# Kernel optimization log

Measured on AMD Instinct MI355X. Metric: run time of the kernel, lower is better.

The kernel has to match this reference:

```python
import jax, jax.numpy as jnp
import numpy as np


def setup_inputs() -> dict:
    key = jax.random.key(0)
    kx, kw = jax.random.split(key)
    x = jax.random.normal(kx, (32, 4096, 1024), dtype=jnp.float32)
    # torch init is rand*0.01 (all-positive, degenerate for sign); use randn*0.01
    # to emulate a trained BNN weight with mixed signs.
    weight = jax.random.normal(kw, (1024, 1024), dtype=jnp.float32) * 0.01
    return {"x": x, "weight": weight}


def reference(x, weight):
    # SignFunction forward: binarize weight to {-1, 0(+at exact 0), +1};
    # torch.sign semantics -> jnp.sign. F.linear(x, W) = x @ W.T
    b_weight = jnp.sign(weight)  # [out, in]
    return jnp.einsum('bsi,oi->bso', x, b_weight)
```

## Files before the change

### kernel.cpp

```cpp
#include <hip/hip_runtime.h>
#include <hip/hip_bf16.h>


typedef __attribute__((ext_vector_type(8))) short bf16x8;
typedef __attribute__((ext_vector_type(4))) float f32x4;

#define BM 128
#define BN 256
#define BK 32
#define KDIM 1024
#define NDIM 1024
#define NKSTEP (KDIM / BK)
#define PADA 40

__device__ __forceinline__ unsigned cvt2(float a, float b) {
  unsigned r;
  asm("v_cvt_pk_bf16_f32 %0, %1, %2" : "=v"(r) : "v"(a), "v"(b));
  return r;
}

__global__ void sign_kernel(const float4* __restrict__ W, ushort4* __restrict__ Bs, int n4) {
  int i = blockIdx.x * blockDim.x + threadIdx.x;
  if (i >= n4) return;
  float4 v = W[i];
  const float* pv = (const float*)&v;
  ushort4 r;
  unsigned short* pr = (unsigned short*)&r;
#pragma unroll
  for (int j = 0; j < 4; ++j) {
    union { float f; unsigned int u; } c; c.f = pv[j];
    pr[j] = ((c.u & 0x7fffffffu) == 0u)
                ? (unsigned short)0
                : (unsigned short)(0x3f80u | ((c.u >> 16) & 0x8000u));
  }
  Bs[i] = r;
}

__global__ __launch_bounds__(256) void bgemm_kernel(
    const float* __restrict__ X,
    const unsigned short* __restrict__ Bs,
    float* __restrict__ O) {
  __shared__ unsigned short sA[2][BM * PADA];
  __shared__ unsigned short sB[2][BN * BK];

  const int t = threadIdx.x;
  const int l = t & 63;
  const int w = t >> 6;
  const int wr = w >> 1;
  const int wc = w & 1;

  const unsigned nwg = gridDim.x;
  unsigned swz = blockIdx.x;
  if ((nwg & 7u) == 0u) swz = (blockIdx.x & 7u) * (nwg >> 3) + (blockIdx.x >> 3);
  const int bm = (int)(swz >> 2);
  const int bn = (int)(swz & 3u);
  const size_t m0 = (size_t)bm * BM;
  const int N0 = bn * BN;

  const int ar = t >> 1;
  const int ah = (t & 1) * 16;
  const float* ag = X + (m0 + (size_t)ar) * KDIM + ah;
  const int aw = ar * PADA + ah;

  const unsigned short* bg[4];
  int bw[4];
#pragma unroll
  for (int i = 0; i < 4; ++i) {
    int c = i * 256 + t;
    int n = c >> 2;
    int q = c & 3;
    int kb2 = q ^ ((n >> 1) & 3);
    bg[i] = Bs + (size_t)(N0 + n) * KDIM + kb2 * 8;
    bw[i] = c * 8;
  }

  const int ll = l & 15;
  const int kb = l >> 4;
  int offA[4], offB[8];
#pragma unroll
  for (int i = 0; i < 4; ++i)
    offA[i] = (wr * 64 + i * 16 + ll) * PADA + kb * 8;
#pragma unroll
  for (int j = 0; j < 8; ++j) {
    int n = wc * 128 + j * 16 + ll;
    int q = kb ^ ((n >> 1) & 3);
    offB[j] = n * BK + q * 8;
  }

  f32x4 acc[4][8];
#pragma unroll
  for (int i = 0; i < 4; ++i)
#pragma unroll
    for (int j = 0; j < 8; ++j) acc[i][j] = (f32x4)0.0f;

#define STAGE(buf, k0)                                                         \
  do {                                                                         \
    _Pragma("unroll") for (int i = 0; i < 4; ++i)                              \
        __builtin_amdgcn_global_load_lds(                                      \
            (const __attribute__((address_space(1))) void*)(bg[i] + (k0)),     \
            (__attribute__((address_space(3))) void*)(&sB[buf][bw[i]]),        \
            16, 0, 0);                                                         \
    const float4* ap = reinterpret_cast<const float4*>(ag + (k0));             \
    float4 v0 = ap[0], v1 = ap[1], v2 = ap[2], v3 = ap[3];                     \
    uint4 lo, hi;                                                              \
    lo.x = cvt2(v0.x, v0.y); lo.y = cvt2(v0.z, v0.w);                          \
    lo.z = cvt2(v1.x, v1.y); lo.w = cvt2(v1.z, v1.w);                          \
    hi.x = cvt2(v2.x, v2.y); hi.y = cvt2(v2.z, v2.w);                          \
    hi.z = cvt2(v3.x, v3.y); hi.w = cvt2(v3.z, v3.w);                          \
    *reinterpret_cast<uint4*>(&sA[buf][aw]) = lo;                              \
    *reinterpret_cast<uint4*>(&sA[buf][aw + 8]) = hi;                          \
  } while (0)

  STAGE(0, 0);
  __syncthreads();

  for (int kk = 0; kk < NKSTEP; ++kk) {
    const int cur = kk & 1;
    if (kk + 1 < NKSTEP) {
      STAGE(cur ^ 1, (kk + 1) * BK);
    }
    const unsigned short* sa = sA[cur];
    const unsigned short* sb = sB[cur];
    bf16x8 av[4];
    bf16x8 bv[8];
#pragma unroll
    for (int i = 0; i < 4; ++i)
      av[i] = *reinterpret_cast<const bf16x8*>(sa + offA[i]);
#pragma unroll
    for (int j = 0; j < 8; ++j)
      bv[j] = *reinterpret_cast<const bf16x8*>(sb + offB[j]);
#pragma unroll
    for (int i = 0; i < 4; ++i)
#pragma unroll
      for (int j = 0; j < 8; ++j)
        acc[i][j] = __builtin_amdgcn_mfma_f32_16x16x32_bf16(av[i], bv[j], acc[i][j], 0, 0, 0);
    __syncthreads();
  }

  const int crow = (l >> 4) * 4;
#pragma unroll
  for (int i = 0; i < 4; ++i) {
    const size_t r0 = m0 + wr * 64 + i * 16 + crow;
#pragma unroll
    for (int j = 0; j < 8; ++j) {
      const int col = N0 + wc * 128 + j * 16 + ll;
      float* op = O + r0 * NDIM + col;
#pragma unroll
      for (int e = 0; e < 4; ++e) op[(size_t)e * NDIM] = acc[i][j][e];
    }
  }
#undef STAGE
}

__global__ void naive_kernel(const float* __restrict__ X, const float* __restrict__ W,
                             float* __restrict__ O, long long total) {
  long long idx = (long long)blockIdx.x * blockDim.x + threadIdx.x;
  if (idx >= total) return;
  int n = (int)(idx & (NDIM - 1));
  long long m = idx >> 10;
  const float* xr = X + m * KDIM;
  const float* wr = W + (long long)n * KDIM;
  float s = 0.f;
  for (int k = 0; k < KDIM; ++k) {
    float wv = wr[k];
    float sg = (wv > 0.f) ? 1.f : ((wv < 0.f) ? -1.f : 0.f);
    s += xr[k] * sg;
  }
  O[idx] = s;
}

extern "C" void kernel_launch(void* const* d_in, const int* in_sizes, int n_in,
                              void* d_out, int out_size, void* d_ws, size_t ws_size,
                              hipStream_t stream) {
  const float* X = (const float*)d_in[0];
  const float* W = (const float*)d_in[1];
  float* O = (float*)d_out;
  const long long M = (long long)in_sizes[0] / KDIM;

  const size_t need_ws = (size_t)NDIM * KDIM * sizeof(unsigned short);
  if (ws_size >= need_ws && (M % BM) == 0) {
    unsigned short* Bs = (unsigned short*)d_ws;
    int n4 = (NDIM * KDIM) / 4;
    sign_kernel<<<dim3(n4 / 256), dim3(256), 0, stream>>>(
        (const float4*)W, (ushort4*)Bs, n4);
    dim3 grid((unsigned)((M / BM) * (NDIM / BN)));
    bgemm_kernel<<<grid, dim3(256), 0, stream>>>(X, Bs, O);
  } else {
    long long total = M * NDIM;
    long long blocks = (total + 255) / 256;
    naive_kernel<<<dim3((unsigned)blocks), dim3(256), 0, stream>>>(X, W, O, total);
  }
}
```

Before: 526.3 us.

## Stage fp32 A tiles directly to LDS and convert on read, single-buffered for occupancy

```diff
diff --git a/kernel.cpp b/kernel.cpp
--- a/kernel.cpp
+++ b/kernel.cpp
@@ -6,12 +6,11 @@
 typedef __attribute__((ext_vector_type(4))) float f32x4;
 
 #define BM 128
-#define BN 256
-#define BK 32
+#define BN 128
+#define BK 64
 #define KDIM 1024
 #define NDIM 1024
 #define NKSTEP (KDIM / BK)
-#define PADA 40
 
 __device__ __forceinline__ unsigned cvt2(float a, float b) {
   unsigned r;
@@ -36,12 +35,12 @@
   Bs[i] = r;
 }
 
-__global__ __launch_bounds__(256) void bgemm_kernel(
+__global__ __launch_bounds__(256, 3) void bgemm_kernel(
     const float* __restrict__ X,
     const unsigned short* __restrict__ Bs,
     float* __restrict__ O) {
-  __shared__ unsigned short sA[2][BM * PADA];
-  __shared__ unsigned short sB[2][BN * BK];
+  __shared__ f32x4 sA[BM * 16];
+  __shared__ unsigned short sB[BN * BK];
 
   const int t = threadIdx.x;
   const int l = t & 63;
@@ -52,104 +51,106 @@
   const unsigned nwg = gridDim.x;
   unsigned swz = blockIdx.x;
   if ((nwg & 7u) == 0u) swz = (blockIdx.x & 7u) * (nwg >> 3) + (blockIdx.x >> 3);
-  const int bm = (int)(swz >> 2);
-  const int bn = (int)(swz & 3u);
+  const int bm = (int)(swz >> 3);
+  const int bn = (int)(swz & 7u);
   const size_t m0 = (size_t)bm * BM;
   const int N0 = bn * BN;
 
-  const int ar = t >> 1;
-  const int ah = (t & 1) * 16;
-  const float* ag = X + (m0 + (size_t)ar) * KDIM + ah;
-  const int aw = ar * PADA + ah;
+  const float* agp[8];
+#pragma unroll
+  for (int i = 0; i < 8; ++i) {
+    int c = i * 256 + t;
+    int r = c >> 4;
+    int q = (c & 15) ^ (r & 15);
+    agp[i] = X + (m0 + (size_t)r) * KDIM + q * 4;
+  }
 
-  const unsigned short* bg[4];
-  int bw[4];
+  const unsigned short* bgp[4];
 #pragma unroll
   for (int i = 0; i < 4; ++i) {
     int c = i * 256 + t;
-    int n = c >> 2;
-    int q = c & 3;
-    int kb2 = q ^ ((n >> 1) & 3);
-    bg[i] = Bs + (size_t)(N0 + n) * KDIM + kb2 * 8;
-    bw[i] = c * 8;
+    int n = c >> 3;
+    int q = (c & 7) ^ (n & 7);
+    bgp[i] = Bs + (size_t)(N0 + n) * KDIM + q * 8;
   }
 
   const int ll = l & 15;
   const int kb = l >> 4;
-  int offA[4], offB[8];
+  int idxA[2][4];
+  int offB[2][4];
 #pragma unroll
-  for (int i = 0; i < 4; ++i)
-    offA[i] = (wr * 64 + i * 16 + ll) * PADA + kb * 8;
+  for (int ks = 0; ks < 2; ++ks) {
 #pragma unroll
-  for (int j = 0; j < 8; ++j) {
-    int n = wc * 128 + j * 16 + ll;
-    int q = kb ^ ((n >> 1) & 3);
-    offB[j] = n * BK + q * 8;
+    for (int i = 0; i < 4; ++i) {
+      int row = wr * 64 + i * 16 + ll;
+      idxA[ks][i] = row * 16 + ((ks * 8 + kb * 2) ^ (row & 15));
+    }
+#pragma unroll
+    for (int j = 0; j < 4; ++j) {
+      int n = wc * 64 + j * 16 + ll;
+      offB[ks][j] = n * 64 + (((ks * 4 + kb) ^ (n & 7)) * 8);
+    }
   }
 
-  f32x4 acc[4][8];
+  f32x4 acc[4][4];
 #pragma unroll
   for (int i = 0; i < 4; ++i)
 #pragma unroll
-    for (int j = 0; j < 8; ++j) acc[i][j] = (f32x4)0.0f;
-
-#define STAGE(buf, k0)                                                         \
-  do {                                                                         \
-    _Pragma("unroll") for (int i = 0; i < 4; ++i)                              \
-        __builtin_amdgcn_global_load_lds(                                      \
-            (const __attribute__((address_space(1))) void*)(bg[i] + (k0)),     \
-            (__attribute__((address_space(3))) void*)(&sB[buf][bw[i]]),        \
-            16, 0, 0);                                                         \
-    const float4* ap = reinterpret_cast<const float4*>(ag + (k0));             \
-    float4 v0 = ap[0], v1 = ap[1], v2 = ap[2], v3 = ap[3];                     \
-    uint4 lo, hi;                                                              \
-    lo.x = cvt2(v0.x, v0.y); lo.y = cvt2(v0.z, v0.w);                          \
-    lo.z = cvt2(v1.x, v1.y); lo.w = cvt2(v1.z, v1.w);                          \
-    hi.x = cvt2(v2.x, v2.y); hi.y = cvt2(v2.z, v2.w);                          \
-    hi.z = cvt2(v3.x, v3.y); hi.w = cvt2(v3.z, v3.w);                          \
-    *reinterpret_cast<uint4*>(&sA[buf][aw]) = lo;                              \
-    *reinterpret_cast<uint4*>(&sA[buf][aw + 8]) = hi;                          \
-  } while (0)
-
-  STAGE(0, 0);
-  __syncthreads();
+    for (int j = 0; j < 4; ++j) acc[i][j] = (f32x4)0.0f;
 
   for (int kk = 0; kk < NKSTEP; ++kk) {
-    const int cur = kk & 1;
-    if (kk + 1 < NKSTEP) {
-      STAGE(cur ^ 1, (kk + 1) * BK);
-    }
-    const unsigned short* sa = sA[cur];
-    const unsigned short* sb = sB[cur];
-    bf16x8 av[4];
-    bf16x8 bv[8];
+    const int k0 = kk * BK;
+#pragma unroll
+    for (int i = 0; i < 8; ++i)
+      __builtin_amdgcn_global_load_lds(
+          (const __attribute__((address_space(1))) void*)(agp[i] + k0),
+          (__attribute__((address_space(3))) void*)(&sA[i * 256 + t]), 16, 0, 0);
 #pragma unroll
     for (int i = 0; i < 4; ++i)
-      av[i] = *reinterpret_cast<const bf16x8*>(sa + offA[i]);
+      __builtin_amdgcn_global_load_lds(
+          (const __attribute__((address_space(1))) void*)(bgp[i] + k0),
+          (__attribute__((address_space(3))) void*)(&sB[(i * 256 + t) * 8]), 16, 0, 0);
+    asm volatile("s_waitcnt vmcnt(0) lgkmcnt(0)" ::: "memory");
+    __syncthreads();
+
 #pragma unroll
-    for (int j = 0; j < 8; ++j)
-      bv[j] = *reinterpret_cast<const bf16x8*>(sb + offB[j]);
+    for (int ks = 0; ks < 2; ++ks) {
+      bf16x8 bv[4];
 #pragma unroll
-    for (int i = 0; i < 4; ++i)
+      for (int j = 0; j < 4; ++j)
+        bv[j] = *reinterpret_cast<const bf16x8*>(sB + offB[ks][j]);
+      bf16x8 av[4];
 #pragma unroll
-      for (int j = 0; j < 8; ++j)
-        acc[i][j] = __builtin_amdgcn_mfma_f32_16x16x32_bf16(av[i], bv[j], acc[i][j], 0, 0, 0);
+      for (int i = 0; i < 4; ++i) {
+        f32x4 c0 = sA[idxA[ks][i]];
+        f32x4 c1 = sA[idxA[ks][i] ^ 1];
+        union { uint4 u; bf16x8 v; } cv;
+        cv.u.x = cvt2(c0.x, c0.y); cv.u.y = cvt2(c0.z, c0.w);
+        cv.u.z = cvt2(c1.x, c1.y); cv.u.w = cvt2(c1.z, c1.w);
+        av[i] = cv.v;
+      }
+#pragma unroll
+      for (int i = 0; i < 4; ++i)
+#pragma unroll
+        for (int j = 0; j < 4; ++j)
+          acc[i][j] = __builtin_amdgcn_mfma_f32_16x16x32_bf16(
+              av[i], bv[j], acc[i][j], 0, 0, 0);
+    }
     __syncthreads();
   }
 
-  const int crow = (l >> 4) * 4;
+  const int crow = kb * 4;
 #pragma unroll
   for (int i = 0; i < 4; ++i) {
     const size_t r0 = m0 + wr * 64 + i * 16 + crow;
 #pragma unroll
-    for (int j = 0; j < 8; ++j) {
-      const int col = N0 + wc * 128 + j * 16 + ll;
+    for (int j = 0; j < 4; ++j) {
+      const int col = N0 + wc * 64 + j * 16 + ll;
       float* op = O + r0 * NDIM + col;
 #pragma unroll
       for (int e = 0; e < 4; ++e) op[(size_t)e * NDIM] = acc[i][j][e];
     }
   }
-#undef STAGE
 }
 
 __global__ void naive_kernel(const float* __restrict__ X, const float* __restrict__ W,
```

Result: faster. 429.1 us (-18.5%).
